# Kernel optimization log

Hardware: AMD Instinct MI355X
Metric: run time of the kernel (lower is better)

Reference implementation:

```python
import jax, jax.numpy as jnp
import numpy as np

B, S, DIM = 4, 3968, 512
H, HD = 8, 64
CHUNK, NPM, MEM = 496, 32, 1024  # MEM == NPM + 2*CHUNK (required by module's EMA update broadcast)


def _lin(k, din, dout):
    kw, kb = jax.random.split(k)
    w = jax.random.normal(kw, (din, dout), jnp.float32) / np.sqrt(din)
    b = jax.random.normal(kb, (dout,), jnp.float32) * 0.01
    return w, b


def setup_inputs() -> dict:
    key = jax.random.key(0)
    ks = jax.random.split(key, 12)
    inp = {}
    inp["x"] = jax.random.normal(ks[0], (B, S, DIM), jnp.float32)
    inp["persistent_memory"] = jax.random.normal(ks[1], (NPM, DIM), jnp.float32)
    # outer query projection
    inp["Wq_out"], inp["bq_out"] = _lin(ks[2], DIM, DIM)
    # NeuralMemory projections
    inp["mk_w"], inp["mk_b"] = _lin(ks[3], DIM, DIM)
    inp["mv_w"], inp["mv_b"] = _lin(ks[4], DIM, DIM)
    inp["mq_w"], inp["mq_b"] = _lin(ks[5], DIM, DIM)
    # TitanAttention (standard MHA: q/k/v to H*HD, out proj back to DIM)
    inp["aq_w"], inp["aq_b"] = _lin(ks[6], DIM, H * HD)
    inp["ak_w"], inp["ak_b"] = _lin(ks[7], DIM, H * HD)
    inp["av_w"], inp["av_b"] = _lin(ks[8], DIM, H * HD)
    inp["ao_w"], inp["ao_b"] = _lin(ks[9], H * HD, DIM)
    return inp


def reference(x, persistent_memory, Wq_out, bq_out,
              mk_w, mk_b, mv_w, mv_b, mq_w, mq_b,
              aq_w, aq_b, ak_w, ak_b, av_w, av_b, ao_w, ao_b):
    Bn, Sn, D = x.shape
    nch = Sn // CHUNK
    inv_sqrt_d = 1.0 / np.sqrt(D).astype(np.float32)
    inv_sqrt_hd = 1.0 / np.sqrt(HD).astype(np.float32)

    def retrieve(mem, q):
        # mem: [B, MEM, D], q: [B, L, D]
        qp = q @ mq_w + mq_b
        k = mem @ mk_w + mk_b
        v = mem @ mv_w + mv_b
        sc = jnp.einsum('bqd,bmd->bqm', qp, k) * inv_sqrt_d
        a = jax.nn.softmax(sc, axis=-1)
        return jnp.einsum('bqm,bmd->bqd', a, v)

    def mha(t):
        # t: [B, L, D] -> [B, L, D]; dropout inactive (eval)
        Bm, L, _ = t.shape
        q = (t @ aq_w + aq_b).reshape(Bm, L, H, HD)
        k = (t @ ak_w + ak_b).reshape(Bm, L, H, HD)
        v = (t @ av_w + av_b).reshape(Bm, L, H, HD)
        sc = jnp.einsum('bqhd,bkhd->bhqk', q, k) * inv_sqrt_hd
        a = jax.nn.softmax(sc, axis=-1)
        o = jnp.einsum('bhqk,bkhd->bqhd', a, v).reshape(Bm, L, H * HD)
        return o @ ao_w + ao_b

    pm = jnp.broadcast_to(persistent_memory[None], (Bn, NPM, D))
    chunks = x.reshape(Bn, nch, CHUNK, D).transpose(1, 0, 2, 3)  # [nch, B, C, D]
    mem0 = jnp.zeros((Bn, MEM, D), x.dtype)

    def step(mem, chunk):
        query = chunk @ Wq_out + bq_out
        hist = retrieve(mem, query)                              # [B, C, D]
        combined = jnp.concatenate([pm, hist, chunk], axis=1)    # [B, MEM, D]
        attended = mha(combined)
        mem2 = 0.9 * mem + 0.1 * attended                        # EMA update
        mout = retrieve(mem2, attended)
        out = (attended * mout)[:, -CHUNK:]                      # keep last chunk slice
        return mem2, out

    _, outs = jax.lax.scan(step, mem0, chunks)                   # outs: [nch, B, C, D]
    return outs.transpose(1, 0, 2, 3).reshape(Bn, Sn, D)
```

## Files before the change

### kernel.cpp

```cpp
#include <hip/hip_runtime.h>
#include <hip/hip_fp16.h>


typedef __attribute__((ext_vector_type(8))) short short8;
typedef __attribute__((ext_vector_type(4))) float f32x4;

static __device__ __forceinline__ unsigned short f32_bf16(float f) {
  unsigned int u = __float_as_uint(f);
  u += 0x7FFFu + ((u >> 16) & 1u);
  return (unsigned short)(u >> 16);
}
static __device__ __forceinline__ float bf_f32(unsigned short h) {
  return __uint_as_float(((unsigned)h) << 16);
}
static __device__ __forceinline__ unsigned pk(float lo, float hi) {
  return (unsigned)f32_bf16(lo) | ((unsigned)f32_bf16(hi) << 16);
}

template<int BM, int BN, int ATY, int BTY, int CTY, bool GUARD, bool BIAS, bool ASPL>
__global__ __launch_bounds__(256) void gemm2(
    const void* __restrict__ Ap, long long Asb, long long Ash, int Ars,
    const void* __restrict__ Bp, long long Bsb, long long Bsh, int Brs,
    void* __restrict__ Cp, long long Csb, long long Csh, int Crs,
    void* __restrict__ Cp2, int csplit, void* __restrict__ Cp3,
    const void* __restrict__ Ap2, long long Asb2,
    const float* __restrict__ bias, float scale, int M, int Kdim, int Hh)
{
  constexpr int LDP = 72;
  constexpr int WN = (BN >= 128) ? 2 : (BM >= 128 ? 1 : 2);
  constexpr int WM = 4 / WN;
  constexpr int MI = BM / (WM * 16);
  constexpr int NI = BN / (WN * 16);
  constexpr int AP = BM / 32;
  constexpr int BP = BN / 32;

  __shared__ unsigned short As[2][BM][LDP];
  __shared__ unsigned short Bs[2][BN][LDP];

  const int tid  = threadIdx.x;
  const int lane = tid & 63;
  const int w    = tid >> 6;
  const int wm   = w / WN, wn = w % WN;
  const int z    = blockIdx.z;
  const int zb   = z / Hh, zh = z - zb * Hh;
  const int m0   = blockIdx.x * BM;
  const int n0   = blockIdx.y * BN;
  const int lrow = lane & 15;
  const int lkB  = (lane >> 4) * 8;
  const int srow = tid >> 3;
  const int scol = (tid & 7) * 8;

  const float*          Af  = (const float*)Ap          + zb * Asb + zh * Ash;
  const unsigned short* Ahp = (const unsigned short*)Ap + zb * Asb + zh * Ash;
  const unsigned short* A2h = (const unsigned short*)Ap2 + zb * Asb2;
  const float*          Bf  = (const float*)Bp          + zb * Bsb + zh * Bsh;
  const unsigned short* Bhp = (const unsigned short*)Bp + zb * Bsb + zh * Bsh;

  float4 afl[AP][2]; uint4 ahl[AP];
  float4 bfl[BP][2]; uint4 bhl[BP];

  auto loadT = [&](int k0) {
    #pragma unroll
    for (int p = 0; p < AP; ++p) {
      const int row = srow + p * 32;
      const int grow = m0 + row;
      const bool ok = !GUARD || grow < M;
      if constexpr (ATY == 0) {
        if (ok) {
          const float* s = Af + (long long)grow * Ars + k0 + scol;
          afl[p][0] = *(const float4*)s;
          afl[p][1] = *(const float4*)(s + 4);
        } else {
          afl[p][0] = make_float4(0.f,0.f,0.f,0.f);
          afl[p][1] = make_float4(0.f,0.f,0.f,0.f);
        }
      } else {
        if (ok) {
          const unsigned short* src;
          if (!ASPL || grow < 496) src = Ahp + (long long)grow * Ars;
          else                     src = A2h + (long long)(grow - 496) * 512;
          ahl[p] = *(const uint4*)(src + k0 + scol);
        } else ahl[p] = make_uint4(0u,0u,0u,0u);
      }
    }
    #pragma unroll
    for (int p = 0; p < BP; ++p) {
      const int row = srow + p * 32;
      if constexpr (BTY == 0) {
        const float* s = Bf + (long long)(n0 + row) * Brs + k0 + scol;
        bfl[p][0] = *(const float4*)s;
        bfl[p][1] = *(const float4*)(s + 4);
      } else {
        bhl[p] = *(const uint4*)(Bhp + (long long)(n0 + row) * Brs + k0 + scol);
      }
    }
  };
  auto writeT = [&](int buf) {
    #pragma unroll
    for (int p = 0; p < AP; ++p) {
      const int row = srow + p * 32;
      uint4 u;
      if constexpr (ATY == 0) {
        u.x = pk(afl[p][0].x, afl[p][0].y); u.y = pk(afl[p][0].z, afl[p][0].w);
        u.z = pk(afl[p][1].x, afl[p][1].y); u.w = pk(afl[p][1].z, afl[p][1].w);
      } else u = ahl[p];
      *(uint4*)(&As[buf][row][scol]) = u;
    }
    #pragma unroll
    for (int p = 0; p < BP; ++p) {
      const int row = srow + p * 32;
      uint4 u;
      if constexpr (BTY == 0) {
        u.x = pk(bfl[p][0].x, bfl[p][0].y); u.y = pk(bfl[p][0].z, bfl[p][0].w);
        u.z = pk(bfl[p][1].x, bfl[p][1].y); u.w = pk(bfl[p][1].z, bfl[p][1].w);
      } else u = bhl[p];
      *(uint4*)(&Bs[buf][row][scol]) = u;
    }
  };

  f32x4 acc[MI][NI] = {};

  loadT(0);
  writeT(0);
  __syncthreads();

  const int NT = Kdim >> 6;
  int cur = 0;
  for (int t = 0; t < NT; ++t) {
    const bool more = (t + 1) < NT;
    if (more) loadT((t + 1) << 6);

    short8 a8[MI][2], b8[NI][2];
    #pragma unroll
    for (int mi = 0; mi < MI; ++mi) {
      const unsigned short* r = &As[cur][wm * (MI * 16) + mi * 16 + lrow][lkB];
      a8[mi][0] = *(const short8*)r;
      a8[mi][1] = *(const short8*)(r + 32);
    }
    #pragma unroll
    for (int ni = 0; ni < NI; ++ni) {
      const unsigned short* r = &Bs[cur][wn * (NI * 16) + ni * 16 + lrow][lkB];
      b8[ni][0] = *(const short8*)r;
      b8[ni][1] = *(const short8*)(r + 32);
    }
    #pragma unroll
    for (int kk = 0; kk < 2; ++kk)
      #pragma unroll
      for (int mi = 0; mi < MI; ++mi)
        #pragma unroll
        for (int ni = 0; ni < NI; ++ni)
          acc[mi][ni] = __builtin_amdgcn_mfma_f32_16x16x32_bf16(a8[mi][kk], b8[ni][kk], acc[mi][ni], 0, 0, 0);

    if (more) writeT(cur ^ 1);
    __syncthreads();
    cur ^= 1;
  }

  float*          Cf  = (float*)Cp          + zb * Csb + zh * Csh;
  unsigned short* Chn = (unsigned short*)Cp + zb * Csb + zh * Csh;
  unsigned short* Ch2 = (unsigned short*)Cp2;
  unsigned short* Kb3 = (unsigned short*)Cp3;
  const bool trside = (CTY == 4 || CTY == 5) ? (n0 >= csplit) : false;

  #pragma unroll
  for (int ni = 0; ni < NI; ++ni) {
    const int col = n0 + wn * (NI * 16) + ni * 16 + lrow;
    const float bv = BIAS ? bias[col] : 0.0f;
    #pragma unroll
    for (int mi = 0; mi < MI; ++mi) {
      const int rbase = m0 + wm * (MI * 16) + mi * 16 + ((lane >> 4) << 2);
      if constexpr (CTY == 5) {
        ushort4 vt;
        #pragma unroll
        for (int r = 0; r < 4; ++r) {
          const int row = rbase + r;
          const float proj = acc[mi][ni][r] * scale + bv;
          const long long midx = (long long)row * Crs + col;
          const float v = 0.9f * Cf[midx] + 0.1f * proj;
          Cf[midx] = v;
          if (!trside) Kb3[(long long)row * 512 + col] = f32_bf16(v);
          else ((unsigned short*)&vt)[r] = f32_bf16(v);
        }
        if (trside)
          *(ushort4*)(&Ch2[(long long)(rbase >> 10) * 524288
                           + (long long)(col - csplit) * 1024 + (rbase & 1023)]) = vt;
      } else if constexpr (CTY == 6) {
        const float* ATTp = (const float*)Cp2;
        float* Of = (float*)Cp;
        #pragma unroll
        for (int r = 0; r < 4; ++r) {
          const int row = rbase + r;
          if (row < M) {
            const float v = acc[mi][ni][r] * scale;
            const float a = ATTp[((long long)zb * 496 + row) * 512 + col];
            Of[((long long)zb * 3968 + (long long)csplit * 496 + row) * 512 + col] = v * a;
          }
        }
      } else if constexpr (CTY == 8) {
        float* ATTo = (float*)Cp2;
        #pragma unroll
        for (int r = 0; r < 4; ++r) {
          const int row = rbase + r;
          if (row < M) {
            const float v = acc[mi][ni][r] * scale + bv;
            if (col < csplit)
              Kb3[((long long)zb * 496 + row) * 512 + col] = f32_bf16(v);
            else
              ATTo[((long long)zb * 496 + row) * 512 + (col - csplit)] = v;
          }
        }
      } else if constexpr (CTY == 9) {
        const float* ATTp = (const float*)Cp2;
        float* Of = (float*)Cp;
        #pragma unroll
        for (int r = 0; r < 4; ++r) {
          const int row = rbase + r;
          if (row < 496) {
            const float v = acc[mi][ni][r] * scale;
            const float a = ATTp[((long long)zb * 496 + row) * 512 + col];
            Of[((long long)zb * 3968 + (long long)csplit * 496 + row) * 512 + col] = v * a;
          } else if (row < M) {
            Kb3[(long long)zb * 524288 + (long long)(32 + row - 496) * 512 + col]
              = f32_bf16(acc[mi][ni][r] * scale);
          }
        }
      } else if (trside) {
        ushort4 v;
        v.x = f32_bf16(acc[mi][ni][0] * scale + bv);
        v.y = f32_bf16(acc[mi][ni][1] * scale + bv);
        v.z = f32_bf16(acc[mi][ni][2] * scale + bv);
        v.w = f32_bf16(acc[mi][ni][3] * scale + bv);
        *(ushort4*)(&Ch2[(long long)(rbase >> 10) * 524288
                         + (long long)(col - csplit) * 1024 + (rbase & 1023)]) = v;
      } else {
        #pragma unroll
        for (int r = 0; r < 4; ++r) {
          const int row = rbase + r;
          if (!GUARD || row < M) {
            const float v = acc[mi][ni][r] * scale + bv;
            if constexpr (CTY == 0)      Cf [(long long)row * Crs + col] = v;
            else                         Chn[(long long)row * Crs + col] = f32_bf16(v);
          }
        }
      }
    }
  }
}

__global__ __launch_bounds__(256) void flash_mha_ks(
    const unsigned short* __restrict__ QK, const unsigned short* __restrict__ Vt,
    unsigned short* __restrict__ Opart, float* __restrict__ ML)
{
  __shared__ unsigned short Ks[128][72];
  __shared__ unsigned short Vs[64][136];
  __shared__ unsigned short Ps[64][136];

  const int tid = threadIdx.x, lane = tid & 63, w = tid >> 6;
  const int f = blockIdx.x;
  const int xcd = f & 7, j = f >> 3;
  const int bh = xcd + 8 * (j >> 5);
  const int jj = j & 31;
  const int qt = jj >> 1, part = jj & 1;
  const int b = bh >> 3, h = bh & 7;
  const int q0 = qt * 64, koff = part * 4;
  const unsigned short* Qp = QK + (long long)b * 1048576 + h * 64;
  const unsigned short* Kp = Qp + 512;
  const unsigned short* Vp = Vt + (long long)b * 524288 + (long long)(h * 64) * 1024;

  const int lr = lane & 15, g = lane >> 4, lk = g * 8;
  const int wq = w * 16;

  short8 qb[2];
  qb[0] = *(const short8*)(Qp + (long long)(q0 + wq + lr) * 1024 + lk);
  qb[1] = *(const short8*)(Qp + (long long)(q0 + wq + lr) * 1024 + 32 + lk);

  const int krow = tid >> 1, kcol = (tid & 1) * 32;
  const int vrow = tid >> 2, vcol = (tid & 3) * 32;

  uint4 kl[4], vl[4];
  auto loadKV = [&](int kt) {
    #pragma unroll
    for (int jx = 0; jx < 4; ++jx)
      kl[jx] = *(const uint4*)(Kp + (long long)(kt * 128 + krow) * 1024 + kcol + jx * 8);
    #pragma unroll
    for (int jx = 0; jx < 4; ++jx)
      vl[jx] = *(const uint4*)(Vp + (long long)vrow * 1024 + kt * 128 + vcol + jx * 8);
  };
  auto writeKV = [&]() {
    #pragma unroll
    for (int jx = 0; jx < 4; ++jx) *(uint4*)(&Ks[krow][kcol + jx * 8]) = kl[jx];
    #pragma unroll
    for (int jx = 0; jx < 4; ++jx) *(uint4*)(&Vs[vrow][vcol + jx * 8]) = vl[jx];
  };

  loadKV(koff); writeKV();
  __syncthreads();

  f32x4 acc[4] = {};
  float m = -1e30f, l = 0.f;

  for (int it = 0; it < 4; ++it) {
    const bool more = it < 3;
    if (more) loadKV(koff + it + 1);

    f32x4 s[8] = {};
    #pragma unroll
    for (int ks = 0; ks < 2; ++ks)
      #pragma unroll
      for (int ni = 0; ni < 8; ++ni) {
        const short8 ka = *(const short8*)(&Ks[ni * 16 + lr][ks * 32 + lk]);
        s[ni] = __builtin_amdgcn_mfma_f32_16x16x32_bf16(ka, qb[ks], s[ni], 0, 0, 0);
      }

    float rm = -1e30f;
    #pragma unroll
    for (int ni = 0; ni < 8; ++ni)
      #pragma unroll
      for (int r = 0; r < 4; ++r) { s[ni][r] *= 0.125f; rm = fmaxf(rm, s[ni][r]); }
    rm = fmaxf(rm, __shfl_xor(rm, 16));
    rm = fmaxf(rm, __shfl_xor(rm, 32));

    const float mn = fmaxf(m, rm);
    const float al = __expf(m - mn);
    m = mn;
    float ls = 0.f;
    #pragma unroll
    for (int ni = 0; ni < 8; ++ni)
      #pragma unroll
      for (int r = 0; r < 4; ++r) { s[ni][r] = __expf(s[ni][r] - m); ls += s[ni][r]; }
    ls += __shfl_xor(ls, 16);
    ls += __shfl_xor(ls, 32);
    l = l * al + ls;
    #pragma unroll
    for (int nd = 0; nd < 4; ++nd)
      #pragma unroll
      for (int r = 0; r < 4; ++r) acc[nd][r] *= al;

    #pragma unroll
    for (int ni = 0; ni < 8; ++ni)
      #pragma unroll
      for (int r = 0; r < 4; ++r)
        Ps[wq + lr][ni * 16 + (g << 2) + r] = f32_bf16(s[ni][r]);

    #pragma unroll
    for (int ks2 = 0; ks2 < 4; ++ks2) {
      const short8 pb = *(const short8*)(&Ps[wq + lr][ks2 * 32 + lk]);
      #pragma unroll
      for (int nd = 0; nd < 4; ++nd) {
        const short8 va = *(const short8*)(&Vs[nd * 16 + lr][ks2 * 32 + lk]);
        acc[nd] = __builtin_amdgcn_mfma_f32_16x16x32_bf16(va, pb, acc[nd], 0, 0, 0);
      }
    }

    if (more) { __syncthreads(); writeKV(); __syncthreads(); }
  }

  const int pbq = (bh * 16 + qt) * 2 + part;
  unsigned short* Ob = Opart + (long long)pbq * 4096;
  #pragma unroll
  for (int nd = 0; nd < 4; ++nd)
    #pragma unroll
    for (int r = 0; r < 4; ++r)
      Ob[(16 * nd + 4 * g + r) * 64 + wq + lr] = f32_bf16(acc[nd][r]);
  if (g == 0) {
    ML[pbq * 128 + wq + lr] = m;
    ML[pbq * 128 + 64 + wq + lr] = l;
  }
}

__global__ __launch_bounds__(256) void combine_mha(
    const unsigned short* __restrict__ Opart, const float* __restrict__ ML,
    unsigned short* __restrict__ OH)
{
  __shared__ float Oc[64][65];
  __shared__ float w1s[64], w2s[64], wis[64];
  const int t = threadIdx.x;
  const int bq = blockIdx.x;
  const int bh = bq >> 4, qt = bq & 15, b = bh >> 3, h = bh & 7, q0 = qt * 64;
  const unsigned short* O1 = Opart + (long long)(bq * 2 + 0) * 4096;
  const unsigned short* O2 = Opart + (long long)(bq * 2 + 1) * 4096;
  const float* ml1 = ML + (bq * 2 + 0) * 128;
  const float* ml2 = ML + (bq * 2 + 1) * 128;
  if (t < 64) {
    const float m1 = ml1[t], l1 = ml1[64 + t], m2 = ml2[t], l2 = ml2[64 + t];
    const float mm = fmaxf(m1, m2);
    const float e1 = __expf(m1 - mm), e2 = __expf(m2 - mm);
    w1s[t] = e1; w2s[t] = e2; wis[t] = 1.0f / (e1 * l1 + e2 * l2);
  }
  __syncthreads();
  {
    const int d = t >> 2, qs = (t & 3) * 16;
    unsigned short ua[16], ub[16];
    *(uint4*)&ua[0] = *(const uint4*)(O1 + d * 64 + qs);
    *(uint4*)&ua[8] = *(const uint4*)(O1 + d * 64 + qs + 8);
    *(uint4*)&ub[0] = *(const uint4*)(O2 + d * 64 + qs);
    *(uint4*)&ub[8] = *(const uint4*)(O2 + d * 64 + qs + 8);
    #pragma unroll
    for (int i = 0; i < 16; ++i) {
      const int q = qs + i;
      Oc[d][q] = (w1s[q] * bf_f32(ua[i]) + w2s[q] * bf_f32(ub[i])) * wis[q];
    }
  }
  __syncthreads();
  {
    const int q = t >> 2, ds = (t & 3) * 16;
    unsigned short tmp[16];
    #pragma unroll
    for (int i = 0; i < 16; ++i) tmp[i] = f32_bf16(Oc[ds + i][q]);
    unsigned short* dst = OH + (long long)b * 524288 + (long long)(q0 + q) * 512 + h * 64 + ds;
    *(uint4*)dst = *(uint4*)&tmp[0];
    *(uint4*)(dst + 8) = *(uint4*)&tmp[8];
  }
}

struct TP7 { const float* s[7]; unsigned short* d[7]; };
__global__ __launch_bounds__(256) void transpose7(TP7 tp)
{
  __shared__ float tile[32][33];
  const float* in = tp.s[blockIdx.z];
  unsigned short* out = tp.d[blockIdx.z];
  const int c0 = blockIdx.x * 32, r0 = blockIdx.y * 32;
  const int xx = threadIdx.x & 31, ys = threadIdx.x >> 5;
  #pragma unroll
  for (int yy = ys; yy < 32; yy += 8)
    tile[yy][xx] = in[(long long)(r0 + yy) * 512 + c0 + xx];
  __syncthreads();
  #pragma unroll
  for (int yy = ys; yy < 32; yy += 8)
    out[(long long)(c0 + yy) * 512 + r0 + xx] = f32_bf16(tile[xx][yy]);
}

__global__ __launch_bounds__(256) void softmax_rows_bf(
    const float* __restrict__ buf, unsigned short* __restrict__ obuf,
    int rowsPerZ, long long zStride)
{
  const int gr   = blockIdx.x * 4 + (threadIdx.x >> 6);
  const int lane = threadIdx.x & 63;
  const int z = gr / rowsPerZ;
  const int i = gr - z * rowsPerZ;
  const float* pf = buf + (long long)z * zStride + (long long)i * 1024 + lane * 16;
  float v[16];
  #pragma unroll
  for (int j = 0; j < 4; ++j) {
    const float4 f = ((const float4*)pf)[j];
    v[4*j+0] = f.x; v[4*j+1] = f.y; v[4*j+2] = f.z; v[4*j+3] = f.w;
  }
  float mx = v[0];
  #pragma unroll
  for (int j = 1; j < 16; ++j) mx = fmaxf(mx, v[j]);
  #pragma unroll
  for (int d = 32; d; d >>= 1) mx = fmaxf(mx, __shfl_xor(mx, d));
  float s = 0.0f;
  #pragma unroll
  for (int j = 0; j < 16; ++j) { v[j] = __expf(v[j] - mx); s += v[j]; }
  #pragma unroll
  for (int d = 32; d; d >>= 1) s += __shfl_xor(s, d);
  const float inv = 1.0f / s;
  unsigned short* ph = obuf + (long long)z * zStride + (long long)i * 1024 + lane * 16;
  unsigned uu[8];
  #pragma unroll
  for (int j = 0; j < 8; ++j) uu[j] = pk(v[2*j] * inv, v[2*j+1] * inv);
  ((uint4*)ph)[0] = make_uint4(uu[0], uu[1], uu[2], uu[3]);
  ((uint4*)ph)[1] = make_uint4(uu[4], uu[5], uu[6], uu[7]);
}

__global__ __launch_bounds__(256) void copy_pm8(const float* __restrict__ pm, unsigned short* __restrict__ comb8)
{
  const int ci = blockIdx.y;
  const int idx = blockIdx.x * 256 + threadIdx.x;
  const int b = idx >> 11, e = idx & 2047;
  const int row = e >> 6, d8 = (e & 63) * 8;
  const float* s = pm + row * 512 + d8;
  const float4 f0 = *(const float4*)s;
  const float4 f1 = *(const float4*)(s + 4);
  uint4 u; u.x = pk(f0.x, f0.y); u.y = pk(f0.z, f0.w); u.z = pk(f1.x, f1.y); u.w = pk(f1.z, f1.w);
  *(uint4*)(comb8 + (long long)ci * 2097152 + (long long)b * 524288 + row * 512 + d8) = u;
}

__global__ __launch_bounds__(256) void copy_chunk8(const float* __restrict__ x, unsigned short* __restrict__ comb8)
{
  const int ci = blockIdx.y;
  const int idx = blockIdx.x * 256 + threadIdx.x;
  const int b = idx / 31744, e = idx % 31744;
  const int row = e >> 6, d8 = (e & 63) * 8;
  const float* s = x + ((long long)b * 3968 + ci * 496 + row) * 512 + d8;
  const float4 f0 = *(const float4*)s;
  const float4 f1 = *(const float4*)(s + 4);
  uint4 u; u.x = pk(f0.x, f0.y); u.y = pk(f0.z, f0.w); u.z = pk(f1.x, f1.y); u.w = pk(f1.z, f1.w);
  *(uint4*)(comb8 + (long long)ci * 2097152 + (long long)b * 524288 + (528 + row) * 512 + d8) = u;
}

__global__ __launch_bounds__(256) void init_kv(const float* __restrict__ mkb, const float* __restrict__ mvb,
                                               float* __restrict__ master, unsigned short* __restrict__ Kb)
{
  const int idx = blockIdx.x * 256 + threadIdx.x;
  const int c4 = (idx & 255) * 4;
  const long long row = idx >> 8;
  const float4 v = *(const float4*)((c4 < 512) ? (mkb + c4) : (mvb + c4 - 512));
  *(float4*)(master + row * 1024 + c4) = v;
  if (c4 < 512) {
    ushort4 h; h.x = f32_bf16(v.x); h.y = f32_bf16(v.y); h.z = f32_bf16(v.z); h.w = f32_bf16(v.w);
    *(ushort4*)(Kb + row * 512 + c4) = h;
  }
}

__global__ __launch_bounds__(256) void init_vt(const float* __restrict__ mvb, unsigned short* __restrict__ VT)
{
  const int idx = blockIdx.x * 256 + threadIdx.x;
  const int k8 = (idx & 127) * 8;
  const int d  = (idx >> 7) & 511;
  const int b  = idx >> 16;
  const unsigned short hv = f32_bf16(mvb[d]);
  const ushort4 h4 = make_ushort4(hv, hv, hv, hv);
  unsigned short* dst = VT + (long long)b * 524288 + (long long)d * 1024 + k8;
  *(ushort4*)dst = h4; *(ushort4*)(dst + 4) = h4;
}

__global__ __launch_bounds__(256) void fuse_bias(const float* __restrict__ bq, const float* __restrict__ mq,
                                                 const float* __restrict__ mqb, float* __restrict__ bqm)
{
  const int c = blockIdx.x * 256 + threadIdx.x;
  float s = mqb[c];
  for (int j = 0; j < 512; ++j) s += bq[j] * mq[j * 512 + c];
  bqm[c] = s;
}

__global__ __launch_bounds__(256) void fuse_bias2(const float* __restrict__ aob,
                                                  const float* __restrict__ mkw, const float* __restrict__ mkb,
                                                  const float* __restrict__ mvw, const float* __restrict__ mvb,
                                                  float* __restrict__ baokv)
{
  const int c = blockIdx.x * 256 + threadIdx.x;
  const float* w  = (c < 512) ? mkw : mvw;
  const float* bb = (c < 512) ? mkb : mvb;
  const int cc = c & 511;
  float s = bb[cc];
  for (int j = 0; j < 512; ++j) s += aob[j] * w[j * 512 + cc];
  baokv[c] = s;
}

extern "C" void kernel_launch(void* const* d_in, const int* in_sizes, int n_in,
                              void* d_out, int out_size, void* d_ws, size_t ws_size,
                              hipStream_t stream)
{
  (void)in_sizes; (void)n_in; (void)out_size; (void)ws_size;
  const float* x   = (const float*)d_in[0];
  const float* pm  = (const float*)d_in[1];
  const float* Wq  = (const float*)d_in[2];
  const float* bq  = (const float*)d_in[3];
  const float* mkw = (const float*)d_in[4];
  const float* mkb = (const float*)d_in[5];
  const float* mvw = (const float*)d_in[6];
  const float* mvb = (const float*)d_in[7];
  const float* mqw = (const float*)d_in[8];
  const float* mqb = (const float*)d_in[9];
  const float* aqw = (const float*)d_in[10];
  const float* aqb = (const float*)d_in[11];
  const float* akw = (const float*)d_in[12];
  const float* akb = (const float*)d_in[13];
  const float* avw = (const float*)d_in[14];
  const float* avb = (const float*)d_in[15];
  const float* aow = (const float*)d_in[16];
  const float* aob = (const float*)d_in[17];
  float* out = (float*)d_out;

  char* wsp = (char*)d_ws;
  size_t off = 0;
  auto alloc = [&](size_t b) -> void* { void* p = wsp + off; off += (b + 255) & ~(size_t)255; return p; };

  unsigned short* WTmq  = (unsigned short*)alloc(524288);
  unsigned short* WKV   = (unsigned short*)alloc(1048576);
  unsigned short* WQKV  = (unsigned short*)alloc(1572864);
  unsigned short* Wqm   = (unsigned short*)alloc(524288);
  unsigned short* WaoKV = (unsigned short*)alloc(1048576);
  unsigned short* WQA   = (unsigned short*)alloc(1048576);
  float* bqkv  = (float*)alloc(6144);
  float* bqm   = (float*)alloc(2048);
  float* baokv = (float*)alloc(4096);
  float* bqa   = (float*)alloc(4096);
  float*          master = (float*)alloc(16777216);
  unsigned short* Kb   = (unsigned short*)alloc(4194304);
  unsigned short* VT   = (unsigned short*)alloc(4194304);
  unsigned short* VTm  = (unsigned short*)alloc(4194304);
  unsigned short* QP1  = (unsigned short*)alloc(16252928);
  unsigned short* QP   = (unsigned short*)alloc(2031616);
  unsigned short* comb8= (unsigned short*)alloc(33554432);
  unsigned short* QKb  = (unsigned short*)alloc(8388608);
  unsigned short* OH   = (unsigned short*)alloc(4194304);
  float*          ATT  = (float*)alloc(4063232);
  float*          SC   = (float*)alloc(16515072);
  unsigned short* SCb  = (unsigned short*)alloc(8257536);
  unsigned short* Opart= (unsigned short*)alloc(8388608);
  float*          ML   = (float*)alloc(524288);

  const long long XBS = 2031616, BS = 524288, QBS = 253952;
  const long long SCB2 = 1015808;
  const float sr = 0.044194173824159216f;

  TP7 tp;
  tp.s[0] = mqw; tp.d[0] = WTmq;
  tp.s[1] = mkw; tp.d[1] = WKV;
  tp.s[2] = mvw; tp.d[2] = WKV + 262144;
  tp.s[3] = aqw; tp.d[3] = WQKV;
  tp.s[4] = akw; tp.d[4] = WQKV + 262144;
  tp.s[5] = avw; tp.d[5] = WQKV + 524288;
  tp.s[6] = aow; tp.d[6] = WQA + 262144;
  transpose7<<<dim3(16,16,7),256,0,stream>>>(tp);
  gemm2<64,64,1,0,2,false,false,false><<<dim3(8,8,1),256,0,stream>>>(
    WTmq, 0, 0, 512, Wq, 0, 0, 512, Wqm, 0, 0, 512,
    nullptr, 0, nullptr, nullptr, 0, nullptr, 1.0f, 512, 512, 1);
  gemm2<64,64,1,0,2,false,false,false><<<dim3(16,8,1),256,0,stream>>>(
    WKV, 0, 0, 512, aow, 0, 0, 512, WaoKV, 0, 0, 512,
    nullptr, 0, nullptr, nullptr, 0, nullptr, 1.0f, 1024, 512, 1);
  gemm2<64,64,1,0,2,false,false,false><<<dim3(8,8,1),256,0,stream>>>(
    WTmq, 0, 0, 512, aow, 0, 0, 512, WQA, 0, 0, 512,
    nullptr, 0, nullptr, nullptr, 0, nullptr, 1.0f, 512, 512, 1);
  fuse_bias<<<2,256,0,stream>>>(bq, mqw, mqb, bqm);
  fuse_bias<<<2,256,0,stream>>>(aob, mqw, mqb, bqa);
  fuse_bias2<<<4,256,0,stream>>>(aob, mkw, mkb, mvw, mvb, baokv);
  hipMemcpyAsync(bqa + 512, aob, 2048, hipMemcpyDeviceToDevice, stream);
  gemm2<128,64,0,1,2,false,true,false><<<dim3(124,8,1),256,0,stream>>>(
    x, 0, 0, 512, Wqm, 0, 0, 512,
    QP1, 0, 0, 512, nullptr, 0, nullptr, nullptr, 0, bqm, 1.0f, 15872, 512, 1);
  hipMemcpyAsync(bqkv,       aqb, 2048, hipMemcpyDeviceToDevice, stream);
  hipMemcpyAsync(bqkv + 512, akb, 2048, hipMemcpyDeviceToDevice, stream);
  hipMemcpyAsync(bqkv +1024, avb, 2048, hipMemcpyDeviceToDevice, stream);
  init_kv<<<4096,256,0,stream>>>(mkb, mvb, master, Kb);
  init_vt<<<1024,256,0,stream>>>(mvb, VT);
  copy_pm8<<<dim3(32,8),256,0,stream>>>(pm, comb8);
  copy_chunk8<<<dim3(496,8),256,0,stream>>>(x, comb8);

  gemm2<64,64,1,1,0,true,false,false><<<dim3(8,16,4),256,0,stream>>>(
    QP1, XBS, 0, 512, Kb, BS, 0, 512,
    SC, SCB2, 0, 1024, nullptr, 0, nullptr, nullptr, 0, nullptr, sr, 496, 512, 1);
  softmax_rows_bf<<<496,256,0,stream>>>(SC, SCb, 496, SCB2);
  gemm2<64,64,1,1,2,true,false,false><<<dim3(8,8,4),256,0,stream>>>(
    SCb, SCB2, 0, 1024, VT, BS, 0, 1024,
    comb8 + 32 * 512, BS, 0, 512, nullptr, 0, nullptr, nullptr, 0, nullptr, 1.0f, 496, 1024, 1);

  for (int ci = 0; ci < 8; ++ci) {
    unsigned short* comb = comb8 + (long long)ci * 2097152;
    const bool last = (ci == 7);
    const int Mm = last ? 496 : 992;

    gemm2<128,64,1,1,4,false,true,false><<<dim3(32,24,1),256,0,stream>>>(
      comb, 0, 0, 512, WQKV, 0, 0, 512,
      QKb, 0, 0, 1024, VTm, 1024, nullptr, nullptr, 0, bqkv, 1.0f, 4096, 512, 1);
    flash_mha_ks<<<1024,256,0,stream>>>(QKb, VTm, Opart, ML);
    combine_mha<<<512,256,0,stream>>>(Opart, ML, OH);

    gemm2<128,64,1,1,5,false,true,false><<<dim3(32,16,1),256,0,stream>>>(
      OH, 0, 0, 512, WaoKV, 0, 0, 512,
      master, 0, 0, 1024, VT, 512, Kb, nullptr, 0, baokv, 1.0f, 4096, 512, 1);
    gemm2<64,64,1,1,8,true,true,false><<<dim3(8,16,4),256,0,stream>>>(
      OH + 528 * 512, BS, 0, 512, WQA, 0, 0, 512,
      nullptr, 0, 0, 512, ATT, 512, QP, nullptr, 0, bqa, 1.0f, 496, 512, 1);

    gemm2<64,64,1,1,0,true,false,true><<<dim3(last?8:16,16,4),256,0,stream>>>(
      QP, QBS, 0, 512, Kb, BS, 0, 512,
      SC, SCB2, 0, 1024, nullptr, 0, nullptr,
      QP1 + (long long)(ci + 1) * 253952, XBS, nullptr, sr, Mm, 512, 1);
    softmax_rows_bf<<<(last?496:992),256,0,stream>>>(SC, SCb, Mm, SCB2);
    gemm2<64,64,1,1,9,true,false,false><<<dim3(last?8:16,8,4),256,0,stream>>>(
      SCb, SCB2, 0, 1024, VT, BS, 0, 1024,
      out, 0, 0, 512, ATT, ci, last ? nullptr : (comb8 + (long long)(ci + 1) * 2097152),
      nullptr, 0, nullptr, 1.0f, Mm, 1024, 1);
  }
}
```

Baseline: 1.251 ms.

## Replace split-KV flash attention plus combine with single-pass flash kernel

Each flash attention block now walks all 8 key tiles itself instead of splitting the keys into two halves. It normalizes by the softmax sum and writes its output tile straight to the head-concatenated buffer through a shared-memory transpose. This removes the combine_mha launch and the partial-output and max/sum buffers along with their memory traffic, at the cost of half as many blocks (512) and a loop twice as long per block. Dead CTY==6 epilogue code is also removed.

```diff
diff --git a/kernel.cpp b/kernel.cpp
--- a/kernel.cpp
+++ b/kernel.cpp
@@ -184,18 +184,6 @@
         if (trside)
           *(ushort4*)(&Ch2[(long long)(rbase >> 10) * 524288
                            + (long long)(col - csplit) * 1024 + (rbase & 1023)]) = vt;
-      } else if constexpr (CTY == 6) {
-        const float* ATTp = (const float*)Cp2;
-        float* Of = (float*)Cp;
-        #pragma unroll
-        for (int r = 0; r < 4; ++r) {
-          const int row = rbase + r;
-          if (row < M) {
-            const float v = acc[mi][ni][r] * scale;
-            const float a = ATTp[((long long)zb * 496 + row) * 512 + col];
-            Of[((long long)zb * 3968 + (long long)csplit * 496 + row) * 512 + col] = v * a;
-          }
-        }
       } else if constexpr (CTY == 8) {
         float* ATTo = (float*)Cp2;
         #pragma unroll
@@ -247,9 +235,9 @@
   }
 }
 
-__global__ __launch_bounds__(256) void flash_mha_ks(
+__global__ __launch_bounds__(256) void flash_mha(
     const unsigned short* __restrict__ QK, const unsigned short* __restrict__ Vt,
-    unsigned short* __restrict__ Opart, float* __restrict__ ML)
+    unsigned short* __restrict__ OH)
 {
   __shared__ unsigned short Ks[128][72];
   __shared__ unsigned short Vs[64][136];
@@ -258,14 +246,14 @@
   const int tid = threadIdx.x, lane = tid & 63, w = tid >> 6;
   const int f = blockIdx.x;
   const int xcd = f & 7, j = f >> 3;
-  const int bh = xcd + 8 * (j >> 5);
-  const int jj = j & 31;
-  const int qt = jj >> 1, part = jj & 1;
+  const int bh = xcd + 8 * (j >> 4);
+  const int qt = j & 15;
   const int b = bh >> 3, h = bh & 7;
-  const int q0 = qt * 64, koff = part * 4;
+  const int q0 = qt * 64;
   const unsigned short* Qp = QK + (long long)b * 1048576 + h * 64;
   const unsigned short* Kp = Qp + 512;
   const unsigned short* Vp = Vt + (long long)b * 524288 + (long long)(h * 64) * 1024;
+  unsigned short* Op = OH + (long long)b * 524288 + h * 64;
 
   const int lr = lane & 15, g = lane >> 4, lk = g * 8;
   const int wq = w * 16;
@@ -280,28 +268,28 @@
   uint4 kl[4], vl[4];
   auto loadKV = [&](int kt) {
     #pragma unroll
-    for (int jx = 0; jx < 4; ++jx)
-      kl[jx] = *(const uint4*)(Kp + (long long)(kt * 128 + krow) * 1024 + kcol + jx * 8);
-    #pragma unroll
-    for (int jx = 0; jx < 4; ++jx)
-      vl[jx] = *(const uint4*)(Vp + (long long)vrow * 1024 + kt * 128 + vcol + jx * 8);
+    for (int jj = 0; jj < 4; ++jj)
+      kl[jj] = *(const uint4*)(Kp + (long long)(kt * 128 + krow) * 1024 + kcol + jj * 8);
+    #pragma unroll
+    for (int jj = 0; jj < 4; ++jj)
+      vl[jj] = *(const uint4*)(Vp + (long long)vrow * 1024 + kt * 128 + vcol + jj * 8);
   };
   auto writeKV = [&]() {
     #pragma unroll
-    for (int jx = 0; jx < 4; ++jx) *(uint4*)(&Ks[krow][kcol + jx * 8]) = kl[jx];
-    #pragma unroll
-    for (int jx = 0; jx < 4; ++jx) *(uint4*)(&Vs[vrow][vcol + jx * 8]) = vl[jx];
+    for (int jj = 0; jj < 4; ++jj) *(uint4*)(&Ks[krow][kcol + jj * 8]) = kl[jj];
+    #pragma unroll
+    for (int jj = 0; jj < 4; ++jj) *(uint4*)(&Vs[vrow][vcol + jj * 8]) = vl[jj];
   };
 
-  loadKV(koff); writeKV();
+  loadKV(0); writeKV();
   __syncthreads();
 
   f32x4 acc[4] = {};
   float m = -1e30f, l = 0.f;
 
-  for (int it = 0; it < 4; ++it) {
-    const bool more = it < 3;
-    if (more) loadKV(koff + it + 1);
+  for (int kt = 0; kt < 8; ++kt) {
+    const bool more = kt < 7;
+    if (more) loadKV(kt + 1);
 
     f32x4 s[8] = {};
     #pragma unroll
@@ -352,65 +340,23 @@
       }
     }
 
-    if (more) { __syncthreads(); writeKV(); __syncthreads(); }
+    __syncthreads();
+    if (more) { writeKV(); __syncthreads(); }
   }
 
-  const int pbq = (bh * 16 + qt) * 2 + part;
-  unsigned short* Ob = Opart + (long long)pbq * 4096;
+  unsigned short (*Os)[72] = (unsigned short (*)[72])&Ks[0][0];
+  const float inv = 1.0f / l;
   #pragma unroll
   for (int nd = 0; nd < 4; ++nd)
     #pragma unroll
     for (int r = 0; r < 4; ++r)
-      Ob[(16 * nd + 4 * g + r) * 64 + wq + lr] = f32_bf16(acc[nd][r]);
-  if (g == 0) {
-    ML[pbq * 128 + wq + lr] = m;
-    ML[pbq * 128 + 64 + wq + lr] = l;
-  }
-}
-
-__global__ __launch_bounds__(256) void combine_mha(
-    const unsigned short* __restrict__ Opart, const float* __restrict__ ML,
-    unsigned short* __restrict__ OH)
-{
-  __shared__ float Oc[64][65];
-  __shared__ float w1s[64], w2s[64], wis[64];
-  const int t = threadIdx.x;
-  const int bq = blockIdx.x;
-  const int bh = bq >> 4, qt = bq & 15, b = bh >> 3, h = bh & 7, q0 = qt * 64;
-  const unsigned short* O1 = Opart + (long long)(bq * 2 + 0) * 4096;
-  const unsigned short* O2 = Opart + (long long)(bq * 2 + 1) * 4096;
-  const float* ml1 = ML + (bq * 2 + 0) * 128;
-  const float* ml2 = ML + (bq * 2 + 1) * 128;
-  if (t < 64) {
-    const float m1 = ml1[t], l1 = ml1[64 + t], m2 = ml2[t], l2 = ml2[64 + t];
-    const float mm = fmaxf(m1, m2);
-    const float e1 = __expf(m1 - mm), e2 = __expf(m2 - mm);
-    w1s[t] = e1; w2s[t] = e2; wis[t] = 1.0f / (e1 * l1 + e2 * l2);
-  }
+      Os[wq + lr][nd * 16 + (g << 2) + r] = f32_bf16(acc[nd][r] * inv);
   __syncthreads();
-  {
-    const int d = t >> 2, qs = (t & 3) * 16;
-    unsigned short ua[16], ub[16];
-    *(uint4*)&ua[0] = *(const uint4*)(O1 + d * 64 + qs);
-    *(uint4*)&ua[8] = *(const uint4*)(O1 + d * 64 + qs + 8);
-    *(uint4*)&ub[0] = *(const uint4*)(O2 + d * 64 + qs);
-    *(uint4*)&ub[8] = *(const uint4*)(O2 + d * 64 + qs + 8);
-    #pragma unroll
-    for (int i = 0; i < 16; ++i) {
-      const int q = qs + i;
-      Oc[d][q] = (w1s[q] * bf_f32(ua[i]) + w2s[q] * bf_f32(ub[i])) * wis[q];
-    }
-  }
-  __syncthreads();
-  {
-    const int q = t >> 2, ds = (t & 3) * 16;
-    unsigned short tmp[16];
-    #pragma unroll
-    for (int i = 0; i < 16; ++i) tmp[i] = f32_bf16(Oc[ds + i][q]);
-    unsigned short* dst = OH + (long long)b * 524288 + (long long)(q0 + q) * 512 + h * 64 + ds;
-    *(uint4*)dst = *(uint4*)&tmp[0];
-    *(uint4*)(dst + 8) = *(uint4*)&tmp[8];
-  }
+  const int orow = tid >> 2, ocol = (tid & 3) * 16;
+  const uint4 u0 = *(const uint4*)(&Os[orow][ocol]);
+  const uint4 u1 = *(const uint4*)(&Os[orow][ocol + 8]);
+  *(uint4*)(Op + (long long)(q0 + orow) * 512 + ocol) = u0;
+  *(uint4*)(Op + (long long)(q0 + orow) * 512 + ocol + 8) = u1;
 }
 
 struct TP7 { const float* s[7]; unsigned short* d[7]; };
@@ -590,8 +536,6 @@
   float*          ATT  = (float*)alloc(4063232);
   float*          SC   = (float*)alloc(16515072);
   unsigned short* SCb  = (unsigned short*)alloc(8257536);
-  unsigned short* Opart= (unsigned short*)alloc(8388608);
-  float*          ML   = (float*)alloc(524288);
 
   const long long XBS = 2031616, BS = 524288, QBS = 253952;
   const long long SCB2 = 1015808;
@@ -646,8 +590,7 @@
     gemm2<128,64,1,1,4,false,true,false><<<dim3(32,24,1),256,0,stream>>>(
       comb, 0, 0, 512, WQKV, 0, 0, 512,
       QKb, 0, 0, 1024, VTm, 1024, nullptr, nullptr, 0, bqkv, 1.0f, 4096, 512, 1);
-    flash_mha_ks<<<1024,256,0,stream>>>(QKb, VTm, Opart, ML);
-    combine_mha<<<512,256,0,stream>>>(Opart, ML, OH);
+    flash_mha<<<512,256,0,stream>>>(QKb, VTm, OH);
 
     gemm2<128,64,1,1,5,false,true,false><<<dim3(32,16,1),256,0,stream>>>(
       OH, 0, 0, 512, WaoKV, 0, 0, 512,
```

Result: faster. 1.215 ms (-2.8%).
